# Kernel optimization log

Hardware: AMD Instinct MI355X
Metric: run time of the kernel (lower is better)

Reference implementation:

```python
import jax, jax.numpy as jnp
import numpy as np

N_NODES = 1_000_000
N_EDGES = 16_000_000
ALPHA = 0.85
MAX_ITER = 100
TOL = 1e-6


def setup_inputs() -> dict:
    key = jax.random.key(0)
    k1, k2 = jax.random.split(key)
    x = jax.random.normal(k1, (N_NODES,), dtype=jnp.float32)
    edge_index = jax.random.randint(k2, (2, N_EDGES), 0, N_NODES, dtype=jnp.int64)
    return {"x": x, "edge_index": edge_index}


def reference(x, edge_index):
    N = x.shape[0]
    rows = edge_index[0]  # destination (row index of sparse M)
    cols = edge_index[1]  # source (column index; out-degree normalization)

    # values of M*alpha: alpha / out_degree(col), gathered per edge
    deg = jax.ops.segment_sum(jnp.ones_like(cols, dtype=jnp.float32), cols,
                              num_segments=N)  # torch.bincount(columns)
    vals = ALPHA / deg[cols]  # [E]; div-by-zero -> inf, matching torch

    inv_n = jnp.float32(1.0) / N
    teleport = (1.0 - ALPHA) * inv_n
    v0 = jnp.full((N,), inv_n, dtype=jnp.float32)
    thresh = jnp.float32(N) * TOL

    def step(carry, _):
        v, done = carry
        # SpMV: out[row] += vals * v[col]
        new_v = jax.ops.segment_sum(vals * v[cols], rows, num_segments=N) + teleport
        err = jnp.abs(new_v - v).sum()
        v_next = jnp.where(done, v, new_v)
        done_next = done | (err < thresh)
        return (v_next, done_next), None

    (v, _), _ = jax.lax.scan(step, (v0, jnp.array(False)), None, length=MAX_ITER)
    return v
```

## Files before the change

### kernel.cpp

```cpp
#include <hip/hip_runtime.h>
#include <hip/hip_cooperative_groups.h>

namespace cg = cooperative_groups;


static constexpr int   NN       = 1000000;
static constexpr int   NE       = 16000000;
static constexpr float ALPHA    = 0.85f;
static constexpr int   MAX_ITER = 100;
static constexpr float THRESH   = 1.0f;
static constexpr float INV_N    = 1.0f / 1000000.0f;
static constexpr float TELEPORT = 0.15f * (1.0f / 1000000.0f);
static constexpr float SCALE    = 8796093022208.0f;
static constexpr float INVSCALE = 1.0f / 8796093022208.0f;

static constexpr int T     = 256;
static constexpr int T5    = 512;
static constexpr int NCH   = 2048;
static constexpr int BSH   = 14;
static constexpr int BKN   = 16384;
static constexpr int NBK   = 64;
static constexpr int NBKU  = 62;
static constexpr int NSUBB = 496;
static constexpr int NSLC  = 489;

static constexpr size_t OFF_WCG  = 0;
static constexpr size_t OFF_COLP = 0;
static constexpr size_t OFF_WRG  = 64002048;
static constexpr size_t OFF_PACC = 96003072;
static constexpr size_t OFF_CNTR = 128508928;
static constexpr size_t OFF_CNTC = 129033216;
static constexpr size_t OFF_CTRL = 129557504;
static constexpr size_t OFF_RDEG = 129561600;
static constexpr size_t OFF_W    = 133561600;
static constexpr size_t NEED     = 137561632;

typedef int      vi4 __attribute__((ext_vector_type(4)));
typedef unsigned vu4 __attribute__((ext_vector_type(4)));

template<typename TT>
__device__ __forceinline__ TT ntload(const TT* p) { return __builtin_nontemporal_load(p); }

struct P {
    unsigned* wcg; unsigned short* colp; unsigned short* wrg;
    int* pacc; unsigned* cntR; unsigned* cntC;
    float* rdeg; float* w;
    unsigned* totR; unsigned* totC; unsigned* baseR; unsigned* baseC;
    unsigned* flags; int* ovf; float* errF;
};
__device__ __forceinline__ P mk(char* ws) {
    P p;
    p.wcg  = (unsigned*)(ws + OFF_WCG);
    p.colp = (unsigned short*)(ws + OFF_COLP);
    p.wrg  = (unsigned short*)(ws + OFF_WRG);
    p.pacc = (int*)(ws + OFF_PACC);
    p.cntR = (unsigned*)(ws + OFF_CNTR);
    p.cntC = (unsigned*)(ws + OFF_CNTC);
    unsigned* ctrl = (unsigned*)(ws + OFF_CTRL);
    p.rdeg = (float*)(ws + OFF_RDEG);
    p.w    = (float*)(ws + OFF_W);
    p.totR = ctrl; p.totC = ctrl + 64; p.baseR = ctrl + 128; p.baseC = ctrl + 200;
    p.flags = ctrl + 280; p.ovf = (int*)(ctrl + 281); p.errF = (float*)(ctrl + 288);
    return p;
}

__device__ void atomic_fallback(cg::grid_group& grid, int is64,
                                const int* e32, const long long* e64,
                                int* ai, int* deg, float* rdeg,
                                float* vA, float* vB, float* w,
                                float* err, float* out,
                                int tid, int stride, int th)
{
    for (int i = tid; i < NN; i += stride) { ai[i] = 0; deg[i] = 0; vA[i] = INV_N; }
    grid.sync();
    if (is64) { const long long* cols = e64 + NE;
        for (int e = tid; e < NE; e += stride) atomicAdd(&deg[(int)cols[e]], 1); }
    else      { const int* cols = e32 + NE;
        for (int e = tid; e < NE; e += stride) atomicAdd(&deg[cols[e]], 1); }
    grid.sync();
    for (int i = tid; i < NN; i += stride) rdeg[i] = ALPHA / (float)deg[i];
    grid.sync();
    float* v = vA; float* nv = vB;
    for (int iter = 0; iter < MAX_ITER; ++iter) {
        for (int i = tid; i < NN; i += stride) { w[i] = v[i] * rdeg[i]; ai[i] = 0; }
        grid.sync();
        if (is64) { const long long* rows = e64; const long long* cols = e64 + NE;
            for (int e = tid; e < NE; e += stride)
                atomicAdd(&ai[(int)rows[e]], __float2int_rn(w[(int)cols[e]] * SCALE)); }
        else { const int* rows = e32; const int* cols = e32 + NE;
            for (int e = tid; e < NE; e += stride)
                atomicAdd(&ai[rows[e]], __float2int_rn(w[cols[e]] * SCALE)); }
        grid.sync();
        float pe = 0.0f;
        for (int i = tid; i < NN; i += stride) {
            float x = TELEPORT + (float)ai[i] * INVSCALE;
            pe += fabsf(x - v[i]); nv[i] = x;
        }
        #pragma unroll
        for (int off = 32; off > 0; off >>= 1) pe += __shfl_down(pe, off, 64);
        if ((th & 63) == 0) unsafeAtomicAdd(&err[iter], pe);
        grid.sync();
        float e = ((volatile float*)err)[iter];
        float* t = v; v = nv; nv = t;
        if (e < THRESH) break;
    }
    for (int i = tid; i < NN; i += stride) out[i] = v[i];
}

__global__ __launch_bounds__(256) void k0_init(const int* __restrict__ e32, char* ws)
{
    P p = mk(ws);
    __shared__ int snz;
    const int th = threadIdx.x;
    if (th == 0) snz = 0;
    __syncthreads();
    if (e32[2 * th + 1] != 0) atomicOr(&snz, 1);
    __syncthreads();
    if (th == 0) { p.flags[0] = (snz == 0) ? 1u : 0u; *p.ovf = 0; p.w[NN] = 0.0f; }
    if (th < MAX_ITER) p.errF[th] = 0.0f;
}

__global__ __launch_bounds__(256, 8) void k1_hist(const int* __restrict__ e32, char* ws)
{
    P p = mk(ws);
    if (p.flags[0]) return;
    __shared__ int h[128];
    const int th = threadIdx.x, blk = blockIdx.x;
    const int e0 = (int)(((long long)NE * blk) >> 11);
    const int e1 = (int)(((long long)NE * (blk + 1)) >> 11);
    if (th < 128) h[th] = 0;
    __syncthreads();
    const vi4* R4 = (const vi4*)e32;
    const vi4* C4 = (const vi4*)(e32 + NE);
    const int qe = (e1 + 3) >> 2;
    for (int q = (e0 >> 2) + th; q < qe; q += T) {
        vi4 R = R4[q], C = C4[q];
        int rr[4] = {R.x, R.y, R.z, R.w}, cc[4] = {C.x, C.y, C.z, C.w};
        #pragma unroll
        for (int j = 0; j < 4; ++j) {
            int e = 4 * q + j;
            if (e >= e0 && e < e1) {
                atomicAdd(&h[rr[j] >> BSH], 1);
                atomicAdd(&h[64 + (cc[j] >> BSH)], 1);
            }
        }
    }
    __syncthreads();
    if (th < 64) {
        p.cntR[(size_t)th * NCH + blk] = (unsigned)h[th];
        p.cntC[(size_t)th * NCH + blk] = (unsigned)h[64 + th];
    }
}

__global__ __launch_bounds__(256, 4) void k2_scan(char* ws)
{
    P p = mk(ws);
    if (p.flags[0]) return;
    __shared__ int S[256];
    const int th = threadIdx.x, blk = blockIdx.x;
    const int side = blk >> 6, b = blk & 63;
    unsigned* cnt = (side ? p.cntC : p.cntR) + (size_t)b * NCH;
    unsigned v[8]; unsigned s = 0;
    #pragma unroll
    for (int i = 0; i < 8; ++i) { v[i] = cnt[8 * th + i]; s += v[i]; }
    S[th] = (int)s; __syncthreads();
    for (int off = 1; off < 256; off <<= 1) {
        int x = (th >= off) ? S[th - off] : 0;
        __syncthreads(); S[th] += x; __syncthreads();
    }
    unsigned run = (unsigned)S[th] - s;
    #pragma unroll
    for (int i = 0; i < 8; ++i) { unsigned t = v[i]; cnt[8 * th + i] = run; run += t; }
    if (th == 255) (side ? p.totC : p.totR)[b] = run;
}

__global__ __launch_bounds__(256) void k2b_bases(char* ws)
{
    P p = mk(ws);
    if (p.flags[0]) return;
    __shared__ int S[128];
    const int th = threadIdx.x;
    unsigned pt = 0;
    if (th < 128) {
        unsigned t = (th < 64) ? p.totR[th] : p.totC[th - 64];
        pt = (t + 7u) & ~7u;
        S[th] = (int)pt;
    }
    __syncthreads();
    for (int off = 1; off < 64; off <<= 1) {
        int x = (th < 128 && (th & 63) >= off) ? S[th - off] : 0;
        __syncthreads(); if (th < 128) S[th] += x; __syncthreads();
    }
    if (th < 64) {
        p.baseR[th] = (unsigned)S[th] - pt;
        if (th == 63) p.baseR[64] = (unsigned)S[63];
    } else if (th < 128) {
        p.baseC[th - 64] = (unsigned)S[th] - pt;
        if (th == 127) p.baseC[64] = (unsigned)S[127];
    }
    __syncthreads();
    if (th < 64) {
        unsigned tot = p.totC[th], bs = p.baseC[th], pp = (tot + 7u) & ~7u;
        for (unsigned i = tot; i < pp; ++i) p.colp[bs + i] = 0;
    }
}

__global__ __launch_bounds__(256, 6) void k3a_col(const int* __restrict__ e32, char* ws)
{
    P p = mk(ws);
    if (p.flags[0]) return;
    __shared__ int SH3[4288];
    unsigned short* pcL = (unsigned short*)SH3;
    int* fills = SH3 + 4096; int* flsh = SH3 + 4160; int* wpos = SH3 + 4224;
    const int th = threadIdx.x, blk = blockIdx.x;
    if (th < 64) { fills[th] = 0; flsh[th] = 0;
                   wpos[th] = (int)(p.baseC[th] + p.cntC[(size_t)th * NCH + blk]); }
    __syncthreads();
    const int e0 = (int)(((long long)NE * blk) >> 11);
    const int e1 = (int)(((long long)NE * (blk + 1)) >> 11);
    const vi4* C4 = (const vi4*)(e32 + NE);
    const int qs = e0 >> 2, qe = (e1 + 3) >> 2;
    vi4 Ccur = {0, 0, 0, 0}; if (qs + th < qe) Ccur = C4[qs + th];
    for (int qb = qs; qb < qe; qb += T) {
        vi4 Cnext = {0, 0, 0, 0};
        { int qn = qb + T + th; if (qn < qe) Cnext = C4[qn]; }
        const int q = qb + th;
        if (q < qe) {
            int cc[4] = {Ccur.x, Ccur.y, Ccur.z, Ccur.w};
            #pragma unroll
            for (int j = 0; j < 4; ++j) {
                int e = 4 * q + j;
                if (e >= e0 && e < e1) {
                    int bb = cc[j] >> BSH;
                    int idx = atomicAdd(&fills[bb], 1);
                    pcL[bb * 128 + (idx & 127)] = (unsigned short)(cc[j] & (BKN - 1));
                }
            }
        }
        __syncthreads();
        const int wv = th >> 6, lane = th & 63;
        for (int k = 0; k < 16; ++k) {
            const int b = wv * 16 + k;
            int ff = fills[b], fl = flsh[b], wp = wpos[b];
            if (ff - fl > 128) *p.ovf = 1;
            while (ff - fl >= 64) {
                p.colp[wp + lane] = pcL[b * 128 + ((fl + lane) & 127)];
                fl += 64; wp += 64;
            }
            if (lane == 0) { flsh[b] = fl; wpos[b] = wp; }
        }
        __syncthreads();
        Ccur = Cnext;
    }
    {
        const int wv = th >> 6, lane = th & 63;
        for (int k = 0; k < 16; ++k) {
            const int b = wv * 16 + k;
            int ff = fills[b], fl = flsh[b], wp = wpos[b];
            while (ff > fl) {
                int n = min(64, ff - fl);
                if (lane < n) p.colp[wp + lane] = pcL[b * 128 + ((fl + lane) & 127)];
                fl += n; wp += n;
            }
        }
    }
}

__global__ __launch_bounds__(256, 2) void k4_deg(char* ws)
{
    P p = mk(ws);
    if (p.flags[0] || *p.ovf) return;
    __shared__ int SH[16384];
    const int th = threadIdx.x, b = blockIdx.x;
    for (int j = th; j < 16384; j += T) SH[j] = 0;
    __syncthreads();
    const unsigned bs = p.baseC[b], tot = p.totC[b], pt = (tot + 7u) & ~7u;
    const unsigned nq = pt >> 3;
    const vu4* p8 = (const vu4*)p.colp + (bs >> 3);
    for (unsigned q = th; q < nq; q += T) {
        vu4 x = ntload(p8 + q);
        atomicAdd(&SH[x.x & 0xFFFFu], 1); atomicAdd(&SH[x.x >> 16], 1);
        atomicAdd(&SH[x.y & 0xFFFFu], 1); atomicAdd(&SH[x.y >> 16], 1);
        atomicAdd(&SH[x.z & 0xFFFFu], 1); atomicAdd(&SH[x.z >> 16], 1);
        atomicAdd(&SH[x.w & 0xFFFFu], 1); atomicAdd(&SH[x.w >> 16], 1);
    }
    __syncthreads();
    if (th == 0) SH[0] -= (int)(pt - tot);
    __syncthreads();
    for (int g = th; g < 4096; g += T) {
        int node = b * BKN + 4 * g;
        if (node < NN) {
            float r0 = ALPHA / (float)SH[4*g+0];
            float r1 = ALPHA / (float)SH[4*g+1];
            float r2 = ALPHA / (float)SH[4*g+2];
            float r3 = ALPHA / (float)SH[4*g+3];
            float4 rr = {r0, r1, r2, r3};
            *(float4*)&p.rdeg[node] = rr;
            float4 ww = {INV_N * r0, INV_N * r1, INV_N * r2, INV_N * r3};
            *(float4*)&p.w[node] = ww;
        }
    }
}

__global__ __launch_bounds__(256, 3) void k3b_row(const int* __restrict__ e32, char* ws)
{
    P p = mk(ws);
    if (p.flags[0] || *p.ovf) return;
    __shared__ int SH3[12480];
    int*            wcL = SH3;
    unsigned short* wrL = (unsigned short*)(SH3 + 8192);
    int* fills = SH3 + 12288; int* flsh = SH3 + 12352; int* wpos = SH3 + 12416;
    const int th = threadIdx.x, blk = blockIdx.x;
    if (blk < 64 && th == 0) {
        unsigned tot = p.totR[blk], bs = p.baseR[blk], pt = (tot + 7u) & ~7u;
        for (unsigned i = tot; i < pt; ++i) { p.wcg[bs + i] = (unsigned)NN; p.wrg[bs + i] = 0; }
    }
    if (th < 64) { fills[th] = 0; flsh[th] = 0;
                   wpos[th] = (int)(p.baseR[th] + p.cntR[(size_t)th * NCH + blk]); }
    __syncthreads();
    const int e0 = (int)(((long long)NE * blk) >> 11);
    const int e1 = (int)(((long long)NE * (blk + 1)) >> 11);
    const vi4* R4 = (const vi4*)e32;
    const vi4* C4 = (const vi4*)(e32 + NE);
    const int qs = e0 >> 2, qe = (e1 + 3) >> 2;
    vi4 Rcur = {0,0,0,0}, Ccur = {0,0,0,0};
    if (qs + th < qe) { Rcur = R4[qs + th]; Ccur = C4[qs + th]; }
    for (int qb = qs; qb < qe; qb += T) {
        vi4 Rnext = {0,0,0,0}, Cnext = {0,0,0,0};
        { int qn = qb + T + th; if (qn < qe) { Rnext = R4[qn]; Cnext = C4[qn]; } }
        const int q = qb + th;
        if (q < qe) {
            int rr[4] = {Rcur.x, Rcur.y, Rcur.z, Rcur.w};
            int cc[4] = {Ccur.x, Ccur.y, Ccur.z, Ccur.w};
            #pragma unroll
            for (int j = 0; j < 4; ++j) {
                int e = 4 * q + j;
                if (e >= e0 && e < e1) {
                    int bb = rr[j] >> BSH;
                    int idx = atomicAdd(&fills[bb], 1);
                    int sl = idx & 127;
                    wcL[bb * 128 + sl] = cc[j];
                    wrL[bb * 128 + sl] = (unsigned short)(rr[j] & (BKN - 1));
                }
            }
        }
        __syncthreads();
        const int wv = th >> 6, lane = th & 63;
        for (int k = 0; k < 16; ++k) {
            const int b = wv * 16 + k;
            int ff = fills[b], fl = flsh[b], wp = wpos[b];
            if (ff - fl > 128) *p.ovf = 1;
            while (ff - fl >= 64) {
                p.wcg[wp + lane] = (unsigned)wcL[b * 128 + ((fl + lane) & 127)];
                p.wrg[wp + lane] = wrL[b * 128 + ((fl + lane) & 127)];
                fl += 64; wp += 64;
            }
            if (lane == 0) { flsh[b] = fl; wpos[b] = wp; }
        }
        __syncthreads();
        Rcur = Rnext; Ccur = Cnext;
    }
    {
        const int wv = th >> 6, lane = th & 63;
        for (int k = 0; k < 16; ++k) {
            const int b = wv * 16 + k;
            int ff = fills[b], fl = flsh[b], wp = wpos[b];
            while (ff > fl) {
                int n = min(64, ff - fl);
                if (lane < n) {
                    p.wcg[wp + lane] = (unsigned)wcL[b * 128 + ((fl + lane) & 127)];
                    p.wrg[wp + lane] = wrL[b * 128 + ((fl + lane) & 127)];
                }
                fl += n; wp += n;
            }
        }
    }
}

#define GATH(G, CA, CB)                              \
    G##0 = w[(unsigned)CA.x]; G##1 = w[(unsigned)CA.y]; \
    G##2 = w[(unsigned)CA.z]; G##3 = w[(unsigned)CA.w]; \
    G##4 = w[(unsigned)CB.x]; G##5 = w[(unsigned)CB.y]; \
    G##6 = w[(unsigned)CB.z]; G##7 = w[(unsigned)CB.w];

#define ATOM(RL, G)                                                         \
    atomicAdd(&SH[RL.x & 0xFFFFu], __float2int_rn(G##0 * SCALE));           \
    atomicAdd(&SH[RL.x >> 16],     __float2int_rn(G##1 * SCALE));           \
    atomicAdd(&SH[RL.y & 0xFFFFu], __float2int_rn(G##2 * SCALE));           \
    atomicAdd(&SH[RL.y >> 16],     __float2int_rn(G##3 * SCALE));           \
    atomicAdd(&SH[RL.z & 0xFFFFu], __float2int_rn(G##4 * SCALE));           \
    atomicAdd(&SH[RL.z >> 16],     __float2int_rn(G##5 * SCALE));           \
    atomicAdd(&SH[RL.w & 0xFFFFu], __float2int_rn(G##6 * SCALE));           \
    atomicAdd(&SH[RL.w >> 16],     __float2int_rn(G##7 * SCALE));

template<int TT>
__device__ __forceinline__ void scatter_phase(const P& p, int* SH, int th, int blk)
{
    const int b = blk >> 3, sub = blk & 7;
    for (int j = th; j < 16384; j += TT) SH[j] = 0;
    __syncthreads();
    const unsigned bs = p.baseR[b], tot = p.totR[b], pt = (tot + 7u) & ~7u;
    const unsigned nq = pt >> 3;
    const unsigned qlo = (nq * (unsigned)sub) >> 3;
    const unsigned qhi = (nq * (unsigned)(sub + 1)) >> 3;
    const vu4* __restrict__ r8 = (const vu4*)p.wrg + (bs >> 3);
    const vi4* __restrict__ c8 = (const vi4*)p.wcg + (bs >> 2);
    const float* __restrict__ w = p.w;

    unsigned q = qlo + th;
    vu4 rlA = {0,0,0,0}, rlB = {0,0,0,0}, rgA = {0,0,0,0}, rgB = {0,0,0,0};
    vi4 caA = {0,0,0,0}, cbA = {0,0,0,0}, caB = {0,0,0,0}, cbB = {0,0,0,0};
    float gA0=0,gA1=0,gA2=0,gA3=0,gA4=0,gA5=0,gA6=0,gA7=0;
    float gB0=0,gB1=0,gB2=0,gB3=0,gB4=0,gB5=0,gB6=0,gB7=0;
    if (q < qhi)      { rlA = ntload(r8+q);      caA = ntload(c8+2*q);        cbA = ntload(c8+2*q+1); }
    if (q + TT < qhi) { rlB = ntload(r8+q+TT);   caB = ntload(c8+2*(q+TT));   cbB = ntload(c8+2*(q+TT)+1); }
    if (q < qhi)      { GATH(gA, caA, cbA); rgA = rlA; }
    while (q < qhi) {
        if (q + TT < qhi)   { GATH(gB, caB, cbB); rgB = rlB; }
        if (q + 2*TT < qhi) { rlA = ntload(r8+q+2*TT); caA = ntload(c8+2*(q+2*TT)); cbA = ntload(c8+2*(q+2*TT)+1); }
        ATOM(rgA, gA);
        q += TT;
        if (q >= qhi) break;
        if (q + TT < qhi)   { GATH(gA, caA, cbA); rgA = rlA; }
        if (q + 2*TT < qhi) { rlB = ntload(r8+q+2*TT); caB = ntload(c8+2*(q+2*TT)); cbB = ntload(c8+2*(q+2*TT)+1); }
        ATOM(rgB, gB);
        q += TT;
    }
    __syncthreads();
    vi4* pa = (vi4*)(p.pacc + (size_t)blk * 16384);
    const vi4* s4 = (const vi4*)SH;
    for (int j = th; j < 4096; j += TT)
        __builtin_nontemporal_store(s4[j], pa + j);
}

__device__ __forceinline__ void merge_phase(const P& p, float* out, int iter,
                                            int th, int blk, float* sred)
{
    float pe = 0.0f;
    const int b = blk >> 3, off = (blk & 7) * 2048;
    for (int g = th; g < 512; g += T) {
        int node = b * BKN + off + 4 * g;
        if (node < NN) {
            vi4 acc = {0, 0, 0, 0};
            #pragma unroll
            for (int qq = 0; qq < 8; ++qq) {
                const vi4* pp = (const vi4*)(p.pacc + (size_t)(b*8+qq)*16384 + off);
                vi4 x = ntload(pp + g);
                acc.x += x.x; acc.y += x.y; acc.z += x.z; acc.w += x.w;
            }
            float x0 = TELEPORT + (float)acc.x * INVSCALE;
            float x1 = TELEPORT + (float)acc.y * INVSCALE;
            float x2 = TELEPORT + (float)acc.z * INVSCALE;
            float x3 = TELEPORT + (float)acc.w * INVSCALE;
            float4 prev;
            if (iter == 0) prev = make_float4(INV_N, INV_N, INV_N, INV_N);
            else           prev = *(const float4*)&out[node];
            pe += fabsf(x0 - prev.x) + fabsf(x1 - prev.y)
                + fabsf(x2 - prev.z) + fabsf(x3 - prev.w);
            float4 nv = {x0, x1, x2, x3};
            *(float4*)&out[node] = nv;
            float4 rd = *(const float4*)&p.rdeg[node];
            float4 nw = {x0*rd.x, x1*rd.y, x2*rd.z, x3*rd.w};
            *(float4*)&p.w[node] = nw;
        }
    }
    #pragma unroll
    for (int o2 = 32; o2 > 0; o2 >>= 1) pe += __shfl_down(pe, o2, 64);
    if ((th & 63) == 0) sred[th >> 6] = pe;
    __syncthreads();
    if (th == 0)
        unsafeAtomicAdd(&p.errF[iter], sred[0] + sred[1] + sred[2] + sred[3]);
}

__global__ __launch_bounds__(512, 2) void k5a_scatter(char* __restrict__ ws)
{
    P p = mk(ws);
    if (p.flags[0] || *p.ovf) return;
    __shared__ int SH[16384];
    scatter_phase<T5>(p, SH, threadIdx.x, blockIdx.x);
}

__global__ __launch_bounds__(256, 4) void k5b_merge(char* __restrict__ ws,
                                                    float* __restrict__ out)
{
    P p = mk(ws);
    if (p.flags[0] || *p.ovf) return;
    __shared__ float sred[4];
    merge_phase(p, out, 0, threadIdx.x, blockIdx.x, sred);
}

__global__ __launch_bounds__(256, 2)
void k5c_iter(const int* __restrict__ e32, const long long* __restrict__ e64,
              char* __restrict__ ws, float* __restrict__ out)
{
    cg::grid_group grid = cg::this_grid();
    P p = mk(ws);
    const int th = threadIdx.x, blk = blockIdx.x;
    const int tid = blk * T + th;
    const int stride = gridDim.x * T;
    __shared__ int SH[16384];
    __shared__ float sred[4];

    if (p.flags[0] || *p.ovf) {
        atomic_fallback(grid, (int)p.flags[0], e32, e64,
                        (int*)ws, (int*)(ws + (size_t)4*1024*1024), p.rdeg,
                        (float*)(ws + (size_t)8*1024*1024),
                        (float*)(ws + (size_t)12*1024*1024),
                        (float*)(ws + (size_t)16*1024*1024),
                        p.errF, out, tid, stride, th);
        return;
    }

    for (int iter = 1; iter < MAX_ITER; ++iter) {
        const float e = ((volatile float*)p.errF)[iter - 1];
        if (e < THRESH) break;
        if (blk < NSUBB) scatter_phase<T>(p, SH, th, blk);
        grid.sync();
        if (blk < NSLC) merge_phase(p, out, iter, th, blk, sred);
        grid.sync();
    }
}

__global__ __launch_bounds__(256, 4)
void pagerank_atomic(const int* __restrict__ e32, const long long* __restrict__ e64,
                     int* __restrict__ ai, int* __restrict__ deg,
                     float* __restrict__ rdeg, float* __restrict__ vA,
                     float* __restrict__ vB, float* __restrict__ w,
                     float* __restrict__ err, int* __restrict__ flags,
                     float* __restrict__ out)
{
    cg::grid_group grid = cg::this_grid();
    const int tid = blockIdx.x * blockDim.x + threadIdx.x;
    const int stride = gridDim.x * blockDim.x;
    if (tid < MAX_ITER) err[tid] = 0.0f;
    if (tid == 0) {
        int nz = 0;
        for (int k = 1; k < 512; k += 2) nz |= e32[k];
        flags[0] = (nz == 0) ? 1 : 0;
    }
    grid.sync();
    atomic_fallback(grid, flags[0], e32, e64, ai, deg, rdeg, vA, vB, w, err, out,
                    tid, stride, threadIdx.x);
}

extern "C" void kernel_launch(void* const* d_in, const int* in_sizes, int n_in,
                              void* d_out, int out_size, void* d_ws, size_t ws_size,
                              hipStream_t stream)
{
    (void)n_in; (void)out_size; (void)in_sizes;
    const int*       e32 = (const int*)d_in[1];
    const long long* e64 = (const long long*)d_in[1];
    float* out = (float*)d_out;
    char*  ws  = (char*)d_ws;

    int occ = 0;
    hipOccupancyMaxActiveBlocksPerMultiprocessor(&occ, (const void*)k5c_iter, T, 0);

    if (ws_size >= NEED && occ >= 2) {
        k0_init<<<1,    T, 0, stream>>>(e32, ws);
        k1_hist<<<NCH,  T, 0, stream>>>(e32, ws);
        k2_scan<<<128,  T, 0, stream>>>(ws);
        k2b_bases<<<1,  T, 0, stream>>>(ws);
        k3a_col<<<NCH,  T, 0, stream>>>(e32, ws);
        k4_deg<<<NBKU,  T, 0, stream>>>(ws);
        k3b_row<<<NCH,  T, 0, stream>>>(e32, ws);
        k5a_scatter<<<NSUBB, T5, 0, stream>>>(ws);
        k5b_merge<<<NSLC, T, 0, stream>>>(ws, out);
        void* args[] = { (void*)&e32, (void*)&e64, (void*)&ws, (void*)&out };
        hipLaunchCooperativeKernel((const void*)k5c_iter,
                                   dim3(512), dim3(T), args, 0, stream);
        return;
    }

    const size_t MB = 1024 * 1024;
    int*   ai    = (int*)(ws);
    int*   deg   = (int*)(ws + 4 * MB);
    float* rdeg  = (float*)(ws + 8 * MB);
    float* vA    = (float*)(ws + 12 * MB);
    float* vB    = (float*)(ws + 16 * MB);
    float* w     = (float*)(ws + 20 * MB);
    float* err   = (float*)(ws + 24 * MB);
    int*   flg   = (int*)(ws + 24 * MB + 4096);
    int occ2 = 0;
    hipOccupancyMaxActiveBlocksPerMultiprocessor(&occ2, (const void*)pagerank_atomic, 256, 0);
    if (occ2 < 1) occ2 = 1;
    int grid = occ2 * 256; if (grid > 2048) grid = 2048;
    void* args[] = { (void*)&e32, (void*)&e64, (void*)&ai, (void*)&deg, (void*)&rdeg,
                     (void*)&vA, (void*)&vB, (void*)&w, (void*)&err, (void*)&flg,
                     (void*)&out };
    hipLaunchCooperativeKernel((const void*)pagerank_atomic,
                               dim3(grid), dim3(256), args, 0, stream);
}
```

Before: 518.8 us.

## Fuse column and row bucketing passes, pack row index bits, split degree histogram

```diff
diff --git a/kernel.cpp b/kernel.cpp
--- a/kernel.cpp
+++ b/kernel.cpp
@@ -23,17 +23,17 @@
 static constexpr int NBKU  = 62;
 static constexpr int NSUBB = 496;
 static constexpr int NSLC  = 489;
+static constexpr int NK4A  = 124;
 
 static constexpr size_t OFF_WCG  = 0;
-static constexpr size_t OFF_COLP = 0;
-static constexpr size_t OFF_WRG  = 64002048;
-static constexpr size_t OFF_PACC = 96003072;
-static constexpr size_t OFF_CNTR = 128508928;
-static constexpr size_t OFF_CNTC = 129033216;
-static constexpr size_t OFF_CTRL = 129557504;
-static constexpr size_t OFF_RDEG = 129561600;
-static constexpr size_t OFF_W    = 133561600;
-static constexpr size_t NEED     = 137561632;
+static constexpr size_t OFF_WR8  = 64002048;
+static constexpr size_t OFF_PACC = 80002560;
+static constexpr size_t OFF_CNTR = 112508416;
+static constexpr size_t OFF_CNTC = 113032704;
+static constexpr size_t OFF_CTRL = 113556992;
+static constexpr size_t OFF_RDEG = 113561088;
+static constexpr size_t OFF_W    = 117561088;
+static constexpr size_t NEED     = 121561120;
 
 typedef int      vi4 __attribute__((ext_vector_type(4)));
 typedef unsigned vu4 __attribute__((ext_vector_type(4)));
@@ -42,7 +42,7 @@
 __device__ __forceinline__ TT ntload(const TT* p) { return __builtin_nontemporal_load(p); }
 
 struct P {
-    unsigned* wcg; unsigned short* colp; unsigned short* wrg;
+    unsigned* wcg; unsigned char* wr8; unsigned short* colp;
     int* pacc; unsigned* cntR; unsigned* cntC;
     float* rdeg; float* w;
     unsigned* totR; unsigned* totC; unsigned* baseR; unsigned* baseC;
@@ -51,8 +51,8 @@
 __device__ __forceinline__ P mk(char* ws) {
     P p;
     p.wcg  = (unsigned*)(ws + OFF_WCG);
-    p.colp = (unsigned short*)(ws + OFF_COLP);
-    p.wrg  = (unsigned short*)(ws + OFF_WRG);
+    p.wr8  = (unsigned char*)(ws + OFF_WR8);
+    p.colp = (unsigned short*)(ws + OFF_PACC);
     p.pacc = (int*)(ws + OFF_PACC);
     p.cntR = (unsigned*)(ws + OFF_CNTR);
     p.cntC = (unsigned*)(ws + OFF_CNTC);
@@ -205,118 +205,27 @@
     }
 }
 
-__global__ __launch_bounds__(256, 6) void k3a_col(const int* __restrict__ e32, char* ws)
+__global__ __launch_bounds__(256, 2) void k3ab_scat(const int* __restrict__ e32, char* ws)
 {
     P p = mk(ws);
     if (p.flags[0]) return;
-    __shared__ int SH3[4288];
-    unsigned short* pcL = (unsigned short*)SH3;
-    int* fills = SH3 + 4096; int* flsh = SH3 + 4160; int* wpos = SH3 + 4224;
-    const int th = threadIdx.x, blk = blockIdx.x;
-    if (th < 64) { fills[th] = 0; flsh[th] = 0;
-                   wpos[th] = (int)(p.baseC[th] + p.cntC[(size_t)th * NCH + blk]); }
-    __syncthreads();
-    const int e0 = (int)(((long long)NE * blk) >> 11);
-    const int e1 = (int)(((long long)NE * (blk + 1)) >> 11);
-    const vi4* C4 = (const vi4*)(e32 + NE);
-    const int qs = e0 >> 2, qe = (e1 + 3) >> 2;
-    vi4 Ccur = {0, 0, 0, 0}; if (qs + th < qe) Ccur = C4[qs + th];
-    for (int qb = qs; qb < qe; qb += T) {
-        vi4 Cnext = {0, 0, 0, 0};
-        { int qn = qb + T + th; if (qn < qe) Cnext = C4[qn]; }
-        const int q = qb + th;
-        if (q < qe) {
-            int cc[4] = {Ccur.x, Ccur.y, Ccur.z, Ccur.w};
-            #pragma unroll
-            for (int j = 0; j < 4; ++j) {
-                int e = 4 * q + j;
-                if (e >= e0 && e < e1) {
-                    int bb = cc[j] >> BSH;
-                    int idx = atomicAdd(&fills[bb], 1);
-                    pcL[bb * 128 + (idx & 127)] = (unsigned short)(cc[j] & (BKN - 1));
-                }
-            }
-        }
-        __syncthreads();
-        const int wv = th >> 6, lane = th & 63;
-        for (int k = 0; k < 16; ++k) {
-            const int b = wv * 16 + k;
-            int ff = fills[b], fl = flsh[b], wp = wpos[b];
-            if (ff - fl > 128) *p.ovf = 1;
-            while (ff - fl >= 64) {
-                p.colp[wp + lane] = pcL[b * 128 + ((fl + lane) & 127)];
-                fl += 64; wp += 64;
-            }
-            if (lane == 0) { flsh[b] = fl; wpos[b] = wp; }
-        }
-        __syncthreads();
-        Ccur = Cnext;
-    }
-    {
-        const int wv = th >> 6, lane = th & 63;
-        for (int k = 0; k < 16; ++k) {
-            const int b = wv * 16 + k;
-            int ff = fills[b], fl = flsh[b], wp = wpos[b];
-            while (ff > fl) {
-                int n = min(64, ff - fl);
-                if (lane < n) p.colp[wp + lane] = pcL[b * 128 + ((fl + lane) & 127)];
-                fl += n; wp += n;
-            }
-        }
-    }
-}
-
-__global__ __launch_bounds__(256, 2) void k4_deg(char* ws)
-{
-    P p = mk(ws);
-    if (p.flags[0] || *p.ovf) return;
-    __shared__ int SH[16384];
-    const int th = threadIdx.x, b = blockIdx.x;
-    for (int j = th; j < 16384; j += T) SH[j] = 0;
-    __syncthreads();
-    const unsigned bs = p.baseC[b], tot = p.totC[b], pt = (tot + 7u) & ~7u;
-    const unsigned nq = pt >> 3;
-    const vu4* p8 = (const vu4*)p.colp + (bs >> 3);
-    for (unsigned q = th; q < nq; q += T) {
-        vu4 x = ntload(p8 + q);
-        atomicAdd(&SH[x.x & 0xFFFFu], 1); atomicAdd(&SH[x.x >> 16], 1);
-        atomicAdd(&SH[x.y & 0xFFFFu], 1); atomicAdd(&SH[x.y >> 16], 1);
-        atomicAdd(&SH[x.z & 0xFFFFu], 1); atomicAdd(&SH[x.z >> 16], 1);
-        atomicAdd(&SH[x.w & 0xFFFFu], 1); atomicAdd(&SH[x.w >> 16], 1);
-    }
-    __syncthreads();
-    if (th == 0) SH[0] -= (int)(pt - tot);
-    __syncthreads();
-    for (int g = th; g < 4096; g += T) {
-        int node = b * BKN + 4 * g;
-        if (node < NN) {
-            float r0 = ALPHA / (float)SH[4*g+0];
-            float r1 = ALPHA / (float)SH[4*g+1];
-            float r2 = ALPHA / (float)SH[4*g+2];
-            float r3 = ALPHA / (float)SH[4*g+3];
-            float4 rr = {r0, r1, r2, r3};
-            *(float4*)&p.rdeg[node] = rr;
-            float4 ww = {INV_N * r0, INV_N * r1, INV_N * r2, INV_N * r3};
-            *(float4*)&p.w[node] = ww;
-        }
-    }
-}
-
-__global__ __launch_bounds__(256, 3) void k3b_row(const int* __restrict__ e32, char* ws)
-{
-    P p = mk(ws);
-    if (p.flags[0] || *p.ovf) return;
-    __shared__ int SH3[12480];
-    int*            wcL = SH3;
-    unsigned short* wrL = (unsigned short*)(SH3 + 8192);
-    int* fills = SH3 + 12288; int* flsh = SH3 + 12352; int* wpos = SH3 + 12416;
+    __shared__ int SH3[14720];
+    unsigned short* pcL  = (unsigned short*)SH3;
+    int*            wcL  = SH3 + 4096;
+    unsigned char*  wr8L = (unsigned char*)(SH3 + 12288);
+    int* cFill = SH3 + 14336; int* cFlsh = SH3 + 14400; int* cWpos = SH3 + 14464;
+    int* rFill = SH3 + 14528; int* rFlsh = SH3 + 14592; int* rWpos = SH3 + 14656;
     const int th = threadIdx.x, blk = blockIdx.x;
     if (blk < 64 && th == 0) {
         unsigned tot = p.totR[blk], bs = p.baseR[blk], pt = (tot + 7u) & ~7u;
-        for (unsigned i = tot; i < pt; ++i) { p.wcg[bs + i] = (unsigned)NN; p.wrg[bs + i] = 0; }
-    }
-    if (th < 64) { fills[th] = 0; flsh[th] = 0;
-                   wpos[th] = (int)(p.baseR[th] + p.cntR[(size_t)th * NCH + blk]); }
+        for (unsigned i = tot; i < pt; ++i) { p.wcg[bs + i] = (unsigned)NN; p.wr8[bs + i] = 0; }
+    }
+    if (th < 64) {
+        cFill[th] = 0; cFlsh[th] = 0;
+        cWpos[th] = (int)(p.baseC[th] + p.cntC[(size_t)th * NCH + blk]);
+        rFill[th] = 0; rFlsh[th] = 0;
+        rWpos[th] = (int)(p.baseR[th] + p.cntR[(size_t)th * NCH + blk]);
+    }
     __syncthreads();
     const int e0 = (int)(((long long)NE * blk) >> 11);
     const int e1 = (int)(((long long)NE * (blk + 1)) >> 11);
@@ -336,11 +245,15 @@
             for (int j = 0; j < 4; ++j) {
                 int e = 4 * q + j;
                 if (e >= e0 && e < e1) {
-                    int bb = rr[j] >> BSH;
-                    int idx = atomicAdd(&fills[bb], 1);
-                    int sl = idx & 127;
-                    wcL[bb * 128 + sl] = cc[j];
-                    wrL[bb * 128 + sl] = (unsigned short)(rr[j] & (BKN - 1));
+                    int cb = cc[j] >> BSH;
+                    int ci = atomicAdd(&cFill[cb], 1);
+                    pcL[cb * 128 + (ci & 127)] = (unsigned short)(cc[j] & (BKN - 1));
+                    int rb = rr[j] >> BSH;
+                    int ri = atomicAdd(&rFill[rb], 1);
+                    int sl = ri & 127;
+                    int rl14 = rr[j] & (BKN - 1);
+                    wcL[rb * 128 + sl]  = (cc[j] & 0xFFFFF) | ((rl14 & 0xFFF) << 20);
+                    wr8L[rb * 128 + sl] = (unsigned char)(rl14 >> 12);
                 }
             }
         }
@@ -348,14 +261,21 @@
         const int wv = th >> 6, lane = th & 63;
         for (int k = 0; k < 16; ++k) {
             const int b = wv * 16 + k;
-            int ff = fills[b], fl = flsh[b], wp = wpos[b];
+            int ff = cFill[b], fl = cFlsh[b], wp = cWpos[b];
+            if (ff - fl > 128) *p.ovf = 1;
+            while (ff - fl >= 64) {
+                p.colp[wp + lane] = pcL[b * 128 + ((fl + lane) & 127)];
+                fl += 64; wp += 64;
+            }
+            if (lane == 0) { cFlsh[b] = fl; cWpos[b] = wp; }
+            ff = rFill[b]; fl = rFlsh[b]; wp = rWpos[b];
             if (ff - fl > 128) *p.ovf = 1;
             while (ff - fl >= 64) {
                 p.wcg[wp + lane] = (unsigned)wcL[b * 128 + ((fl + lane) & 127)];
-                p.wrg[wp + lane] = wrL[b * 128 + ((fl + lane) & 127)];
+                p.wr8[wp + lane] = wr8L[b * 128 + ((fl + lane) & 127)];
                 fl += 64; wp += 64;
             }
-            if (lane == 0) { flsh[b] = fl; wpos[b] = wp; }
+            if (lane == 0) { rFlsh[b] = fl; rWpos[b] = wp; }
         }
         __syncthreads();
         Rcur = Rnext; Ccur = Cnext;
@@ -364,12 +284,18 @@
         const int wv = th >> 6, lane = th & 63;
         for (int k = 0; k < 16; ++k) {
             const int b = wv * 16 + k;
-            int ff = fills[b], fl = flsh[b], wp = wpos[b];
+            int ff = cFill[b], fl = cFlsh[b], wp = cWpos[b];
+            while (ff > fl) {
+                int n = min(64, ff - fl);
+                if (lane < n) p.colp[wp + lane] = pcL[b * 128 + ((fl + lane) & 127)];
+                fl += n; wp += n;
+            }
+            ff = rFill[b]; fl = rFlsh[b]; wp = rWpos[b];
             while (ff > fl) {
                 int n = min(64, ff - fl);
                 if (lane < n) {
                     p.wcg[wp + lane] = (unsigned)wcL[b * 128 + ((fl + lane) & 127)];
-                    p.wrg[wp + lane] = wrL[b * 128 + ((fl + lane) & 127)];
+                    p.wr8[wp + lane] = wr8L[b * 128 + ((fl + lane) & 127)];
                 }
                 fl += n; wp += n;
             }
@@ -377,21 +303,94 @@
     }
 }
 
-#define GATH(G, CA, CB)                              \
-    G##0 = w[(unsigned)CA.x]; G##1 = w[(unsigned)CA.y]; \
-    G##2 = w[(unsigned)CA.z]; G##3 = w[(unsigned)CA.w]; \
-    G##4 = w[(unsigned)CB.x]; G##5 = w[(unsigned)CB.y]; \
-    G##6 = w[(unsigned)CB.z]; G##7 = w[(unsigned)CB.w];
-
-#define ATOM(RL, G)                                                         \
-    atomicAdd(&SH[RL.x & 0xFFFFu], __float2int_rn(G##0 * SCALE));           \
-    atomicAdd(&SH[RL.x >> 16],     __float2int_rn(G##1 * SCALE));           \
-    atomicAdd(&SH[RL.y & 0xFFFFu], __float2int_rn(G##2 * SCALE));           \
-    atomicAdd(&SH[RL.y >> 16],     __float2int_rn(G##3 * SCALE));           \
-    atomicAdd(&SH[RL.z & 0xFFFFu], __float2int_rn(G##4 * SCALE));           \
-    atomicAdd(&SH[RL.z >> 16],     __float2int_rn(G##5 * SCALE));           \
-    atomicAdd(&SH[RL.w & 0xFFFFu], __float2int_rn(G##6 * SCALE));           \
-    atomicAdd(&SH[RL.w >> 16],     __float2int_rn(G##7 * SCALE));
+__global__ __launch_bounds__(256, 2) void k4a_deg(char* ws, float* __restrict__ outp)
+{
+    P p = mk(ws);
+    if (p.flags[0] || *p.ovf) return;
+    __shared__ int SH[16384];
+    const int th = threadIdx.x, blk = blockIdx.x;
+    const int b = blk >> 1, sub = blk & 1;
+    for (int j = th; j < 16384; j += T) SH[j] = 0;
+    __syncthreads();
+    const unsigned bs = p.baseC[b], tot = p.totC[b], pt = (tot + 7u) & ~7u;
+    const unsigned nq = pt >> 3;
+    const unsigned qlo = (nq * (unsigned)sub) >> 1;
+    const unsigned qhi = (nq * (unsigned)(sub + 1)) >> 1;
+    const vu4* p8 = (const vu4*)p.colp + (bs >> 3);
+    for (unsigned q = qlo + th; q < qhi; q += T) {
+        vu4 x = ntload(p8 + q);
+        atomicAdd(&SH[x.x & 0xFFFFu], 1); atomicAdd(&SH[x.x >> 16], 1);
+        atomicAdd(&SH[x.y & 0xFFFFu], 1); atomicAdd(&SH[x.y >> 16], 1);
+        atomicAdd(&SH[x.z & 0xFFFFu], 1); atomicAdd(&SH[x.z >> 16], 1);
+        atomicAdd(&SH[x.w & 0xFFFFu], 1); atomicAdd(&SH[x.w >> 16], 1);
+    }
+    __syncthreads();
+    unsigned* hp = (unsigned*)((unsigned short*)outp + (size_t)blk * 16384);
+    for (int j = th; j < 8192; j += T)
+        __builtin_nontemporal_store(
+            (unsigned)((SH[2*j] & 0xFFFF) | (SH[2*j+1] << 16)), hp + j);
+}
+
+__global__ __launch_bounds__(256, 8) void k4b_merge(char* ws, const float* __restrict__ outp)
+{
+    P p = mk(ws);
+    if (p.flags[0] || *p.ovf) return;
+    const int th = threadIdx.x, blk = blockIdx.x;
+    const int b = blk >> 3, off = (blk & 7) * 2048;
+    const int padC = (int)(((p.totC[b] + 7u) & ~7u) - p.totC[b]);
+    const unsigned* h0 = (const unsigned*)((const unsigned short*)outp
+                         + (size_t)(2*b) * 16384 + off);
+    const unsigned* h1 = (const unsigned*)((const unsigned short*)outp
+                         + (size_t)(2*b+1) * 16384 + off);
+    for (int g = th; g < 512; g += T) {
+        int node = b * BKN + off + 4 * g;
+        if (node < NN) {
+            unsigned a0 = ntload(h0 + 2*g), a1 = ntload(h0 + 2*g + 1);
+            unsigned b0 = ntload(h1 + 2*g), b1 = ntload(h1 + 2*g + 1);
+            int d0 = (int)((a0 & 0xFFFFu) + (b0 & 0xFFFFu));
+            int d1 = (int)((a0 >> 16) + (b0 >> 16));
+            int d2 = (int)((a1 & 0xFFFFu) + (b1 & 0xFFFFu));
+            int d3 = (int)((a1 >> 16) + (b1 >> 16));
+            if (off == 0 && g == 0) d0 -= padC;
+            float r0 = ALPHA / (float)d0;
+            float r1 = ALPHA / (float)d1;
+            float r2 = ALPHA / (float)d2;
+            float r3 = ALPHA / (float)d3;
+            float4 rr = {r0, r1, r2, r3};
+            *(float4*)&p.rdeg[node] = rr;
+            float4 ww = {INV_N * r0, INV_N * r1, INV_N * r2, INV_N * r3};
+            *(float4*)&p.w[node] = ww;
+        }
+    }
+}
+
+#define GATH8(G, I, CA, CB, H)                                              \
+    G##0 = w[(unsigned)CA.x & 0xFFFFFu];                                    \
+    G##1 = w[(unsigned)CA.y & 0xFFFFFu];                                    \
+    G##2 = w[(unsigned)CA.z & 0xFFFFFu];                                    \
+    G##3 = w[(unsigned)CA.w & 0xFFFFFu];                                    \
+    G##4 = w[(unsigned)CB.x & 0xFFFFFu];                                    \
+    G##5 = w[(unsigned)CB.y & 0xFFFFFu];                                    \
+    G##6 = w[(unsigned)CB.z & 0xFFFFFu];                                    \
+    G##7 = w[(unsigned)CB.w & 0xFFFFFu];                                    \
+    I##0 = ((unsigned)CA.x >> 20) | ((unsigned)( (H)        & 3ull) << 12); \
+    I##1 = ((unsigned)CA.y >> 20) | ((unsigned)(((H) >> 8)  & 3ull) << 12); \
+    I##2 = ((unsigned)CA.z >> 20) | ((unsigned)(((H) >> 16) & 3ull) << 12); \
+    I##3 = ((unsigned)CA.w >> 20) | ((unsigned)(((H) >> 24) & 3ull) << 12); \
+    I##4 = ((unsigned)CB.x >> 20) | ((unsigned)(((H) >> 32) & 3ull) << 12); \
+    I##5 = ((unsigned)CB.y >> 20) | ((unsigned)(((H) >> 40) & 3ull) << 12); \
+    I##6 = ((unsigned)CB.z >> 20) | ((unsigned)(((H) >> 48) & 3ull) << 12); \
+    I##7 = ((unsigned)CB.w >> 20) | ((unsigned)(((H) >> 56) & 3ull) << 12);
+
+#define ATOM8(I, G)                                                         \
+    atomicAdd(&SH[I##0], __float2int_rn(G##0 * SCALE));                     \
+    atomicAdd(&SH[I##1], __float2int_rn(G##1 * SCALE));                     \
+    atomicAdd(&SH[I##2], __float2int_rn(G##2 * SCALE));                     \
+    atomicAdd(&SH[I##3], __float2int_rn(G##3 * SCALE));                     \
+    atomicAdd(&SH[I##4], __float2int_rn(G##4 * SCALE));                     \
+    atomicAdd(&SH[I##5], __float2int_rn(G##5 * SCALE));                     \
+    atomicAdd(&SH[I##6], __float2int_rn(G##6 * SCALE));                     \
+    atomicAdd(&SH[I##7], __float2int_rn(G##7 * SCALE));
 
 template<int TT>
 __device__ __forceinline__ void scatter_phase(const P& p, int* SH, int th, int blk)
@@ -403,27 +402,30 @@
     const unsigned nq = pt >> 3;
     const unsigned qlo = (nq * (unsigned)sub) >> 3;
     const unsigned qhi = (nq * (unsigned)(sub + 1)) >> 3;
-    const vu4* __restrict__ r8 = (const vu4*)p.wrg + (bs >> 3);
     const vi4* __restrict__ c8 = (const vi4*)p.wcg + (bs >> 2);
+    const unsigned long long* __restrict__ h8 =
+        (const unsigned long long*)(p.wr8 + bs);
     const float* __restrict__ w = p.w;
 
     unsigned q = qlo + th;
-    vu4 rlA = {0,0,0,0}, rlB = {0,0,0,0}, rgA = {0,0,0,0}, rgB = {0,0,0,0};
     vi4 caA = {0,0,0,0}, cbA = {0,0,0,0}, caB = {0,0,0,0}, cbB = {0,0,0,0};
+    unsigned long long hA = 0, hB = 0;
     float gA0=0,gA1=0,gA2=0,gA3=0,gA4=0,gA5=0,gA6=0,gA7=0;
     float gB0=0,gB1=0,gB2=0,gB3=0,gB4=0,gB5=0,gB6=0,gB7=0;
-    if (q < qhi)      { rlA = ntload(r8+q);      caA = ntload(c8+2*q);        cbA = ntload(c8+2*q+1); }
-    if (q + TT < qhi) { rlB = ntload(r8+q+TT);   caB = ntload(c8+2*(q+TT));   cbB = ntload(c8+2*(q+TT)+1); }
-    if (q < qhi)      { GATH(gA, caA, cbA); rgA = rlA; }
+    unsigned iA0=0,iA1=0,iA2=0,iA3=0,iA4=0,iA5=0,iA6=0,iA7=0;
+    unsigned iB0=0,iB1=0,iB2=0,iB3=0,iB4=0,iB5=0,iB6=0,iB7=0;
+    if (q < qhi)      { caA = ntload(c8+2*q);      cbA = ntload(c8+2*q+1);      hA = ntload(h8+q); }
+    if (q + TT < qhi) { caB = ntload(c8+2*(q+TT)); cbB = ntload(c8+2*(q+TT)+1); hB = ntload(h8+q+TT); }
+    if (q < qhi)      { GATH8(gA, iA, caA, cbA, hA) }
     while (q < qhi) {
-        if (q + TT < qhi)   { GATH(gB, caB, cbB); rgB = rlB; }
-        if (q + 2*TT < qhi) { rlA = ntload(r8+q+2*TT); caA = ntload(c8+2*(q+2*TT)); cbA = ntload(c8+2*(q+2*TT)+1); }
-        ATOM(rgA, gA);
+        if (q + TT < qhi)   { GATH8(gB, iB, caB, cbB, hB) }
+        if (q + 2*TT < qhi) { caA = ntload(c8+2*(q+2*TT)); cbA = ntload(c8+2*(q+2*TT)+1); hA = ntload(h8+q+2*TT); }
+        ATOM8(iA, gA)
         q += TT;
         if (q >= qhi) break;
-        if (q + TT < qhi)   { GATH(gA, caA, cbA); rgA = rlA; }
-        if (q + 2*TT < qhi) { rlB = ntload(r8+q+2*TT); caB = ntload(c8+2*(q+2*TT)); cbB = ntload(c8+2*(q+2*TT)+1); }
-        ATOM(rgB, gB);
+        if (q + TT < qhi)   { GATH8(gA, iA, caA, cbA, hA) }
+        if (q + 2*TT < qhi) { caB = ntload(c8+2*(q+2*TT)); cbB = ntload(c8+2*(q+2*TT)+1); hB = ntload(h8+q+2*TT); }
+        ATOM8(iB, gB)
         q += TT;
     }
     __syncthreads();
@@ -561,9 +563,9 @@
         k1_hist<<<NCH,  T, 0, stream>>>(e32, ws);
         k2_scan<<<128,  T, 0, stream>>>(ws);
         k2b_bases<<<1,  T, 0, stream>>>(ws);
-        k3a_col<<<NCH,  T, 0, stream>>>(e32, ws);
-        k4_deg<<<NBKU,  T, 0, stream>>>(ws);
-        k3b_row<<<NCH,  T, 0, stream>>>(e32, ws);
+        k3ab_scat<<<NCH, T, 0, stream>>>(e32, ws);
+        k4a_deg<<<NK4A, T, 0, stream>>>(ws, out);
+        k4b_merge<<<NSLC, T, 0, stream>>>(ws, out);
         k5a_scatter<<<NSUBB, T5, 0, stream>>>(ws);
         k5b_merge<<<NSLC, T, 0, stream>>>(ws, out);
         void* args[] = { (void*)&e32, (void*)&e64, (void*)&ws, (void*)&out };
```

Result: slower. 545.3 us (+5.1%).
